# Kernel optimization log

Hardware: AMD Instinct MI355X
Metric: run time of the kernel (lower is better)

Reference implementation:

```python
import jax, jax.numpy as jnp
import numpy as np

STRIDES = (8, 16, 32)
FMP = ((160, 160), (80, 80), (40, 40))
NUM_CLASSES = 80
TOPK = 1000
CONF_THRESH = 0.05
NMS_THRESH = 0.6
IMG_MAX = 1280.0
CLASS_OFFSET = 8192.0  # > any box coordinate, separates classes for batched NMS


def setup_inputs() -> dict:
    key = jax.random.key(0)
    ks = jax.random.split(key, 32)
    C = 256
    inp = {}
    for l, (h, w) in enumerate(FMP):
        inp[f'feat{l}'] = jax.random.normal(ks[l], (1, C, h, w), dtype=jnp.float32)
        inp[f'Wobj{l}'] = jax.random.normal(ks[3 + 6 * l + 0], (1, C), dtype=jnp.float32) * 0.05
        inp[f'bobj{l}'] = jnp.zeros((1,), dtype=jnp.float32)
        inp[f'Wcls{l}'] = jax.random.normal(ks[3 + 6 * l + 2], (NUM_CLASSES, C), dtype=jnp.float32) * 0.05
        inp[f'bcls{l}'] = jnp.zeros((NUM_CLASSES,), dtype=jnp.float32)
        inp[f'Wreg{l}'] = jax.random.normal(ks[3 + 6 * l + 4], (4, C), dtype=jnp.float32) * 0.05
        inp[f'breg{l}'] = jnp.zeros((4,), dtype=jnp.float32)
    return inp


def _level(feat, Wo, bo, Wc, bc, Wr, br, stride):
    x = feat[0]  # [C,H,W]
    H, W = x.shape[1], x.shape[2]
    def conv1x1(Wm, bv):
        # 1x1 conv == channel GEMM; output [H*W, O]
        return (jnp.einsum('oc,chw->hwo', Wm, x) + bv).reshape(H * W, -1)
    obj = conv1x1(Wo, bo)              # [M,1]
    cls = conv1x1(Wc, bc)              # [M,C]
    reg = jnp.exp(conv1x1(Wr, br)) * stride  # [M,4] (l,t,r,b)
    prob = jax.nn.sigmoid(obj) * jax.nn.sigmoid(cls)
    scores = prob.max(axis=-1)
    labels = prob.argmax(axis=-1)
    ay, ax = jnp.meshgrid(jnp.arange(H), jnp.arange(W), indexing='ij')
    anchors = (jnp.stack([ax, ay], axis=-1).astype(jnp.float32).reshape(-1, 2) + 0.5) * stride
    k = min(TOPK, H * W)
    scores, idx = jax.lax.top_k(scores, k)
    labels = labels[idx]
    reg = reg[idx]
    anchors = anchors[idx]
    boxes = jnp.concatenate([anchors - reg[:, :2], anchors + reg[:, 2:]], axis=-1)
    return scores, labels, boxes


def _batched_nms(boxes, scores, labels):
    N = boxes.shape[0]
    valid = scores >= CONF_THRESH
    # class-offset trick: per-class NMS == single NMS on disjoint offset boxes
    ob = boxes + labels.astype(boxes.dtype)[:, None] * CLASS_OFFSET
    order = jnp.argsort(-scores)
    b = ob[order]
    v = valid[order]
    x1, y1, x2, y2 = b[:, 0], b[:, 1], b[:, 2], b[:, 3]
    areas = (x2 - x1) * (y2 - y1)
    xx1 = jnp.maximum(x1[:, None], x1[None, :])
    yy1 = jnp.maximum(y1[:, None], y1[None, :])
    xx2 = jnp.minimum(x2[:, None], x2[None, :])
    yy2 = jnp.minimum(y2[:, None], y2[None, :])
    w = jnp.maximum(1e-10, xx2 - xx1)
    h = jnp.maximum(1e-10, yy2 - yy1)
    inter = w * h
    iou = inter / (areas[:, None] + areas[None, :] - inter + 1e-14)
    idxs = jnp.arange(N)
    def body(i, keep):
        sup = keep[i] & (iou[i] > NMS_THRESH) & (idxs > i)
        return keep & ~sup
    keep_sorted = jax.lax.fori_loop(0, N, body, v)
    keep = jnp.zeros(N, dtype=bool).at[order].set(keep_sorted)
    return keep


def reference(feat0, feat1, feat2,
              Wobj0, bobj0, Wcls0, bcls0, Wreg0, breg0,
              Wobj1, bobj1, Wcls1, bcls1, Wreg1, breg1,
              Wobj2, bobj2, Wcls2, bcls2, Wreg2, breg2):
    feats = (feat0, feat1, feat2)
    params = ((Wobj0, bobj0, Wcls0, bcls0, Wreg0, breg0),
              (Wobj1, bobj1, Wcls1, bcls1, Wreg1, breg1),
              (Wobj2, bobj2, Wcls2, bcls2, Wreg2, breg2))
    ss, ll, bb = [], [], []
    for l in range(3):
        s, lab, box = _level(feats[l], *params[l], STRIDES[l])
        ss.append(s); ll.append(lab); bb.append(box)
    scores = jnp.concatenate(ss)
    labels = jnp.concatenate(ll)
    boxes = jnp.concatenate(bb)
    keep = _batched_nms(boxes, scores, labels)
    bboxes = jnp.clip(boxes / IMG_MAX, 0.0, 1.0)
    return bboxes, scores, labels.astype(jnp.int32), keep
```

## Files before the change

kernel.cpp:

```cpp
#include <hip/hip_runtime.h>
#include <math.h>

#define NTOT   33600
#define NSEL   3000
#define CAND_CAP 8192
#define NWORDS 47
#define NROWS_PAD 3008
#define FCAP 4

struct P21 {
  const float* feat[3];
  const float* Wobj[3];
  const float* bobj[3];
  const float* Wcls[3];
  const float* bcls[3];
  const float* Wreg[3];
  const float* breg[3];
};

__device__ __forceinline__ void level_of_block(int b, int t, int& l, int& p, int& g,
                                               int& HW, int& Wd, double& stride) {
  if (b < 100)      { l = 0; p = b * 256 + t;         g = p;          HW = 25600; Wd = 160; stride = 8.0;  }
  else if (b < 125) { l = 1; p = (b - 100) * 256 + t; g = 25600 + p;  HW = 6400;  Wd = 80;  stride = 16.0; }
  else              { l = 2; p = (b - 125) * 256 + t; g = 32000 + p;  HW = 1600;  Wd = 40;  stride = 32.0; }
}

__device__ __forceinline__ double sigmoid_d(double x) { return 1.0 / (1.0 + exp(-x)); }

__device__ __forceinline__ unsigned long long shfl64(unsigned long long v, int src) {
  unsigned lo = (unsigned)__shfl((int)(unsigned)(v & 0xFFFFFFFFull), src, 64);
  unsigned hi = (unsigned)__shfl((int)(unsigned)(v >> 32), src, 64);
  return (((unsigned long long)hi) << 32) | (unsigned long long)lo;
}

__global__ __launch_bounds__(256) void k_conv_chunk(P21 P,
    double* __restrict__ obj_t, double* __restrict__ reg_t,
    double* __restrict__ cmax, int* __restrict__ clab) {
  int l, p, g, HW, Wd; double stride;
  level_of_block(blockIdx.x, threadIdx.x, l, p, g, HW, Wd, stride);
  if (p >= HW) return;
  const int chunk = blockIdx.y;
  const float* __restrict__ fp = P.feat[l] + p;

  if (chunk == 0) {
    const float* __restrict__ Wobj = P.Wobj[l];
    const float* __restrict__ Wreg = P.Wreg[l];
    double accO = (double)P.bobj[l][0];
    double accR[4];
#pragma unroll
    for (int j = 0; j < 4; j++) accR[j] = (double)P.breg[l][j];
    for (int c = 0; c < 256; c += 8) {
      double xc[8];
#pragma unroll
      for (int u = 0; u < 8; u++) xc[u] = (double)fp[(c + u) * HW];
#pragma unroll
      for (int u = 0; u < 8; u++) {
        accO = fma((double)Wobj[c + u], xc[u], accO);
#pragma unroll
        for (int j = 0; j < 4; j++)
          accR[j] = fma((double)Wreg[j * 256 + c + u], xc[u], accR[j]);
      }
    }
    obj_t[g] = accO;
#pragma unroll
    for (int j = 0; j < 4; j++) reg_t[4 * g + j] = accR[j];
  } else {
    const int base = (chunk - 1) * 16;
    const float* __restrict__ Wcls = P.Wcls[l];
    const float* __restrict__ bcls = P.bcls[l];
    double a[16];
#pragma unroll
    for (int j = 0; j < 16; j++) a[j] = (double)bcls[base + j];
    for (int c = 0; c < 256; c += 8) {
      double xc[8];
#pragma unroll
      for (int u = 0; u < 8; u++) xc[u] = (double)fp[(c + u) * HW];
#pragma unroll
      for (int u = 0; u < 8; u++) {
#pragma unroll
        for (int j = 0; j < 16; j++)
          a[j] = fma((double)Wcls[(base + j) * 256 + c + u], xc[u], a[j]);
      }
    }
    double maxv = a[0]; int lab = base;
#pragma unroll
    for (int j = 1; j < 16; j++) if (a[j] > maxv) { maxv = a[j]; lab = base + j; }
    cmax[(chunk - 1) * NTOT + g] = maxv;
    clab[(chunk - 1) * NTOT + g] = lab;
  }
}

__global__ __launch_bounds__(256) void k_combine(
    const double* __restrict__ obj_t, const double* __restrict__ reg_t,
    const double* __restrict__ cmax, const int* __restrict__ clab,
    double* __restrict__ score_d, int* __restrict__ label_d,
    double* __restrict__ box_d, unsigned* __restrict__ hist) {
  int l, p, g, HW, Wd; double stride;
  level_of_block(blockIdx.x, threadIdx.x, l, p, g, HW, Wd, stride);
  if (p >= HW) return;

  double maxv = cmax[g]; int lab = clab[g];
#pragma unroll
  for (int k = 1; k < 5; k++) {
    double v = cmax[k * NTOT + g];
    int lb = clab[k * NTOT + g];
    if (v > maxv) { maxv = v; lab = lb; }
  }
  double score = sigmoid_d(obj_t[g]) * sigmoid_d(maxv);
  int h = p / Wd, w = p - h * Wd;
  double ax = ((double)w + 0.5) * stride;
  double ay = ((double)h + 0.5) * stride;
  double e0 = exp(reg_t[4 * g + 0]) * stride;
  double e1 = exp(reg_t[4 * g + 1]) * stride;
  double e2 = exp(reg_t[4 * g + 2]) * stride;
  double e3 = exp(reg_t[4 * g + 3]) * stride;

  score_d[g] = score;
  label_d[g] = lab;
  box_d[4 * g + 0] = ax - e0;
  box_d[4 * g + 1] = ay - e1;
  box_d[4 * g + 2] = ax + e2;
  box_d[4 * g + 3] = ay + e3;

  unsigned key = __float_as_uint((float)score);
  atomicAdd(&hist[l * 65536 + (key >> 16)], 1u);
}

__global__ __launch_bounds__(256) void k_scan(const unsigned* __restrict__ hist,
                                              unsigned* __restrict__ cutB) {
  int l = blockIdx.x;
  const unsigned* h = hist + l * 65536;
  __shared__ unsigned cs[256];
  __shared__ unsigned hb[256];
  __shared__ int s_chunk;
  __shared__ unsigned s_acc;
  int t = threadIdx.x;
  unsigned s = 0;
  for (int b = 0; b < 256; b++) s += h[t * 256 + b];
  cs[t] = s;
  __syncthreads();
  if (t == 0) {
    unsigned acc = 0; int chunk = 0;
    for (int tt = 255; tt >= 0; tt--) {
      if (acc + cs[tt] >= 1000u) { chunk = tt; break; }
      acc += cs[tt];
    }
    s_chunk = chunk; s_acc = acc;
  }
  __syncthreads();
  int chunk = s_chunk;
  hb[t] = h[chunk * 256 + t];
  __syncthreads();
  if (t == 0) {
    unsigned acc = s_acc;
    unsigned B = (unsigned)(chunk * 256);
    for (int b = 255; b >= 0; b--) {
      unsigned c = hb[b];
      if (acc + c >= 1000u) { B = (unsigned)(chunk * 256 + b); break; }
      acc += c;
    }
    cutB[l] = B;
  }
}

__global__ __launch_bounds__(256) void k_compact(const double* __restrict__ score_d,
    const unsigned* __restrict__ cutB, unsigned* __restrict__ cnt,
    double* __restrict__ cand_s, int* __restrict__ cand_g) {
  int l, p, g, HW, Wd; double stride;
  level_of_block(blockIdx.x, threadIdx.x, l, p, g, HW, Wd, stride);
  if (p >= HW) return;
  double sc = score_d[g];
  unsigned key = __float_as_uint((float)sc);
  if ((key >> 16) >= cutB[l]) {
    unsigned pos = atomicAdd(&cnt[l], 1u);
    if (pos < CAND_CAP) {
      cand_s[l * CAND_CAP + pos] = sc;
      cand_g[l * CAND_CAP + pos] = g;
    }
  }
}

__global__ __launch_bounds__(256) void k_rank(const double* __restrict__ cand_s,
    const int* __restrict__ cand_g, const unsigned* __restrict__ cnt,
    const int* __restrict__ label_d, const double* __restrict__ box_d,
    double* __restrict__ sel_s, int* __restrict__ sel_lab, double* __restrict__ sel_box) {
  const int l = blockIdx.y;
  const int M = (int)min(cnt[l], (unsigned)CAND_CAP);
  if (blockIdx.x * 4 >= M) return;
  const int q = blockIdx.x * 4 + (threadIdx.x >> 6);
  const int lane = threadIdx.x & 63;
  const bool active = (q < M);

  double s = 0.0; int g = 0;
  if (active) { s = cand_s[l * CAND_CAP + q]; g = cand_g[l * CAND_CAP + q]; }

  int r = 0;
  if (active) {
    for (int j = lane; j < M; j += 64) {
      double sj = cand_s[l * CAND_CAP + j];
      int gj = cand_g[l * CAND_CAP + j];
      r += (sj > s) || (sj == s && gj < g);
    }
  }
#pragma unroll
  for (int off = 32; off > 0; off >>= 1) r += __shfl_down(r, off, 64);

  if (active && lane == 0 && r < 1000) {
    int o = l * 1000 + r;
    sel_s[o] = s;
    sel_lab[o] = label_d[g];
    sel_box[4 * o + 0] = box_d[4 * g + 0];
    sel_box[4 * o + 1] = box_d[4 * g + 1];
    sel_box[4 * o + 2] = box_d[4 * g + 2];
    sel_box[4 * o + 3] = box_d[4 * g + 3];
  }
}

__global__ __launch_bounds__(256) void k_order(const double* __restrict__ sel_s,
                                               int* __restrict__ sortIdx) {
  const int i = blockIdx.x;
  const int t = threadIdx.x;
  const double s = sel_s[i];
  int r = 0;
  for (int j = t; j < NSEL; j += 256) {
    double sj = sel_s[j];
    r += (sj > s) || (sj == s && j < i);
  }
#pragma unroll
  for (int off = 32; off > 0; off >>= 1) r += __shfl_down(r, off, 64);
  __shared__ int wsum[4];
  if ((t & 63) == 0) wsum[t >> 6] = r;
  __syncthreads();
  if (t == 0) sortIdx[wsum[0] + wsum[1] + wsum[2] + wsum[3]] = i;
}

__global__ __launch_bounds__(256) void k_build(const double* __restrict__ sel_s,
    const int* __restrict__ sel_lab, const double* __restrict__ sel_box,
    const int* __restrict__ sortIdx, double* __restrict__ sbox, int* __restrict__ svalid) {
  int r = blockIdx.x * 256 + threadIdx.x;
  if (r >= NSEL) return;
  int i = sortIdx[r];
  double off = (double)sel_lab[i] * 8192.0;
  sbox[4 * r + 0] = sel_box[4 * i + 0] + off;
  sbox[4 * r + 1] = sel_box[4 * i + 1] + off;
  sbox[4 * r + 2] = sel_box[4 * i + 2] + off;
  sbox[4 * r + 3] = sel_box[4 * i + 3] + off;
  svalid[r] = (sel_s[i] >= 0.05) ? 1 : 0;
}

__global__ __launch_bounds__(64) void k_mask(const double* __restrict__ sbox,
    unsigned long long* __restrict__ denseG, unsigned long long* __restrict__ diagG,
    unsigned short* __restrict__ entG, unsigned short* __restrict__ cntG) {
  int i = blockIdx.x;
  int lane = threadIdx.x;
  double x1 = sbox[4 * i + 0], y1 = sbox[4 * i + 1];
  double x2 = sbox[4 * i + 2], y2 = sbox[4 * i + 3];
  double ar = (x2 - x1) * (y2 - y1);
  int iw = i >> 6;
  unsigned long long myw = 0ull, dg = 0ull;
  int cnt = 0;
  for (int w = 0; w < NWORDS; w++) {
    int j = w * 64 + lane;
    bool c = false;
    if (j < NSEL && j > i) {
      double bx1 = sbox[4 * j + 0], by1 = sbox[4 * j + 1];
      double bx2 = sbox[4 * j + 2], by2 = sbox[4 * j + 3];
      double arj = (bx2 - bx1) * (by2 - by1);
      double xx1 = fmax(x1, bx1), yy1 = fmax(y1, by1);
      double xx2 = fmin(x2, bx2), yy2 = fmin(y2, by2);
      double ww = fmax(1e-10, xx2 - xx1);
      double hh = fmax(1e-10, yy2 - yy1);
      double inter = ww * hh;
      double iou = inter / (ar + arj - inter + 1e-14);
      c = iou > 0.6;
    }
    unsigned long long word = __ballot(c);
    if (lane == w) myw = word;
    if (w == iw) dg = word;
    if (w > iw && lane == 0) {
      unsigned long long t = word;
      while (t) {
        int b = __builtin_ctzll(t); t &= t - 1;
        if (cnt < FCAP) entG[i * FCAP + cnt] = (unsigned short)(w * 64 + b);
        cnt++;
      }
    }
  }
  if (lane < NWORDS) denseG[(size_t)i * 48 + lane] = myw;
  if (lane == 0) { diagG[i] = dg; cntG[i] = (unsigned short)cnt; }
}

__global__ __launch_bounds__(256) void k_nms_scan(
    const unsigned long long* __restrict__ denseG, const unsigned long long* __restrict__ diagG,
    const unsigned short* __restrict__ entG, const unsigned short* __restrict__ cntG,
    const int* __restrict__ svalid, const int* __restrict__ sortIdx,
    int* __restrict__ keepOrig) {
  __shared__ unsigned long long diagL[NROWS_PAD];
  __shared__ unsigned short entL[NROWS_PAD * FCAP];
  __shared__ unsigned short cntL[NROWS_PAD];
  __shared__ unsigned long long validL[48];
  __shared__ unsigned long long hasWL[48];
  const int t = threadIdx.x;
  const int lane = t & 63;

  for (int i = t; i < NROWS_PAD; i += 256) {
    diagL[i] = (i < NSEL) ? diagG[i] : 0ull;
    cntL[i]  = (i < NSEL) ? cntG[i] : (unsigned short)0;
  }
  for (int k = t; k < NSEL * FCAP; k += 256) entL[k] = entG[k];
  for (int k = t + NSEL * FCAP; k < NROWS_PAD * FCAP; k += 256) entL[k] = 0;
  for (int i0 = t; i0 < NROWS_PAD; i0 += 256) {
    bool f = (i0 < NSEL) && (svalid[i0] != 0);
    unsigned long long b = __ballot(f);
    if ((t & 63) == 0) validL[i0 >> 6] = b;
  }
  __syncthreads();
  if (t >= 64) return;

  for (int w = 0; w < NWORDS; w++) {
    int i = w * 64 + lane;
    bool f = (diagL[i] != 0ull) || (cntL[i] != 0);
    unsigned long long b = __ballot(f);
    if (lane == 0) hasWL[w] = b;
  }

  unsigned long long rem = 0ull;
  unsigned long long keep = 0ull;
  for (int w = 0; w < NWORDS; w++) {
    unsigned long long vw = validL[w];
    unsigned long long remw = shfl64(rem, w);
    unsigned long long win = vw & ~remw;
    unsigned long long work = hasWL[w];
    while (work) {
      int d = __builtin_ctzll(work); work &= work - 1;
      if ((win >> d) & 1ull) {
        int i = w * 64 + d;
        win &= ~diagL[i];
        int c = cntL[i];
        if (c > FCAP) {
          unsigned long long rowj = (lane < NWORDS) ? denseG[(size_t)i * 48 + lane] : 0ull;
          rem |= rowj;
        } else {
          for (int k = 0; k < c; k++) {
            int j = entL[i * FCAP + k];
            if ((j >> 6) == lane) rem |= 1ull << (j & 63);
          }
        }
      }
    }
    if (lane == w) keep = win;
  }
  if (lane < NWORDS) {
    for (int b = 0; b < 64; b++) {
      int j = lane * 64 + b;
      if (j < NSEL) keepOrig[sortIdx[j]] = (int)((keep >> b) & 1ull);
    }
  }
}

__global__ __launch_bounds__(256) void k_out(const double* __restrict__ sel_s,
    const int* __restrict__ sel_lab, const double* __restrict__ sel_box,
    const int* __restrict__ keepOrig, float* __restrict__ out) {
  int i = blockIdx.x * 256 + threadIdx.x;
  if (i >= NSEL) return;
#pragma unroll
  for (int c = 0; c < 4; c++) {
    double v = sel_box[4 * i + c] / 1280.0;
    v = fmin(fmax(v, 0.0), 1.0);
    out[4 * i + c] = (float)v;
  }
  out[12000 + i] = (float)sel_s[i];
  out[15000 + i] = (float)sel_lab[i];
  out[18000 + i] = keepOrig[i] ? 1.0f : 0.0f;
}

extern "C" void kernel_launch(void* const* d_in, const int* in_sizes, int n_in,
                              void* d_out, int out_size, void* d_ws, size_t ws_size,
                              hipStream_t stream) {
  P21 P;
  for (int l = 0; l < 3; l++) {
    P.feat[l] = (const float*)d_in[7 * l + 0];
    P.Wobj[l] = (const float*)d_in[7 * l + 1];
    P.bobj[l] = (const float*)d_in[7 * l + 2];
    P.Wcls[l] = (const float*)d_in[7 * l + 3];
    P.bcls[l] = (const float*)d_in[7 * l + 4];
    P.Wreg[l] = (const float*)d_in[7 * l + 5];
    P.breg[l] = (const float*)d_in[7 * l + 6];
  }

  char* ws = (char*)d_ws;
  size_t off = 0;
  auto alloc = [&](size_t bytes) -> char* {
    char* p = ws + off;
    off += (bytes + 15) & ~(size_t)15;
    return p;
  };
  double* score_d  = (double*)alloc((size_t)NTOT * 8);
  double* box_d    = (double*)alloc((size_t)NTOT * 4 * 8);
  int*    label_d  = (int*)   alloc((size_t)NTOT * 4);
  double* obj_t    = (double*)alloc((size_t)NTOT * 8);
  double* reg_t    = (double*)alloc((size_t)NTOT * 4 * 8);
  double* cmax     = (double*)alloc((size_t)5 * NTOT * 8);
  int*    clab     = (int*)   alloc((size_t)5 * NTOT * 4);
  double* sel_s    = (double*)alloc((size_t)NSEL * 8);
  double* sel_box  = (double*)alloc((size_t)NSEL * 4 * 8);
  int*    sel_lab  = (int*)   alloc((size_t)NSEL * 4);
  int*    sortIdx  = (int*)   alloc((size_t)NSEL * 4);
  double* sbox     = (double*)alloc((size_t)NSEL * 4 * 8);
  int*    svalid   = (int*)   alloc((size_t)NSEL * 4);
  int*    keepOrig = (int*)   alloc((size_t)NSEL * 4);
  double* cand_s   = (double*)alloc((size_t)3 * CAND_CAP * 8);
  int*    cand_g   = (int*)   alloc((size_t)3 * CAND_CAP * 4);
  unsigned long long* denseG = (unsigned long long*)alloc((size_t)NSEL * 48 * 8);
  unsigned long long* diagG  = (unsigned long long*)alloc((size_t)NSEL * 8);
  unsigned short*     entG   = (unsigned short*)alloc((size_t)NSEL * FCAP * 2);
  unsigned short*     cntG   = (unsigned short*)alloc((size_t)NSEL * 2);
  unsigned* hist   = (unsigned*)alloc((size_t)3 * 65536 * 4);
  unsigned* cnt    = (unsigned*)alloc(16);
  unsigned* cutB   = (unsigned*)alloc(16);

  hipMemsetAsync(hist, 0, (size_t)3 * 65536 * 4 + 16, stream);

  dim3 cgrid(132, 6, 1);
  k_conv_chunk<<<cgrid, 256, 0, stream>>>(P, obj_t, reg_t, cmax, clab);
  k_combine <<<132, 256, 0, stream>>>(obj_t, reg_t, cmax, clab, score_d, label_d, box_d, hist);
  k_scan    <<<3, 256, 0, stream>>>(hist, cutB);
  k_compact <<<132, 256, 0, stream>>>(score_d, cutB, cnt, cand_s, cand_g);
  dim3 rgrid(CAND_CAP / 4, 3, 1);
  k_rank    <<<rgrid, 256, 0, stream>>>(cand_s, cand_g, cnt, label_d, box_d,
                                        sel_s, sel_lab, sel_box);
  k_order   <<<NSEL, 256, 0, stream>>>(sel_s, sortIdx);
  k_build   <<<(NSEL + 255) / 256, 256, 0, stream>>>(sel_s, sel_lab, sel_box, sortIdx, sbox, svalid);
  k_mask    <<<NSEL, 64, 0, stream>>>(sbox, denseG, diagG, entG, cntG);
  k_nms_scan<<<1, 256, 0, stream>>>(denseG, diagG, entG, cntG, svalid, sortIdx, keepOrig);
  k_out     <<<(NSEL + 255) / 256, 256, 0, stream>>>(sel_s, sel_lab, sel_box, keepOrig, (float*)d_out);
}
```

Baseline: 302.4 us.

## Split channel reduction across waves, parallelize histogram scan and IoU mask rows

The 1x1-conv kernel now gives each block 64 pixels and splits the 256 channels across four waves, reducing partial sums through shared memory. This gives 4x more blocks so more of the GPU is busy. The histogram memset is folded into the conv kernel and the serial per-thread histogram scan becomes a parallel wave-reduction kernel. The NMS mask kernel uses four waves per row. The nms_scan loads are vectorized. Risks are extra shared-memory sync and reduction overhead, and summation order changing from sequential to four partial sums, which could flip near-tie argmax or top-k results.

```diff
diff --git a/kernel.cpp b/kernel.cpp
--- a/kernel.cpp
+++ b/kernel.cpp
@@ -7,6 +7,8 @@
 #define NWORDS 47
 #define NROWS_PAD 3008
 #define FCAP 4
+#define NGRP 525
+#define HISTZ_N 196612
 
 struct P21 {
   const float* feat[3];
@@ -18,11 +20,11 @@
   const float* breg[3];
 };
 
-__device__ __forceinline__ void level_of_block(int b, int t, int& l, int& p, int& g,
+__device__ __forceinline__ void level_of_group(int grp, int lane, int& l, int& p, int& g,
                                                int& HW, int& Wd, double& stride) {
-  if (b < 100)      { l = 0; p = b * 256 + t;         g = p;          HW = 25600; Wd = 160; stride = 8.0;  }
-  else if (b < 125) { l = 1; p = (b - 100) * 256 + t; g = 25600 + p;  HW = 6400;  Wd = 80;  stride = 16.0; }
-  else              { l = 2; p = (b - 125) * 256 + t; g = 32000 + p;  HW = 1600;  Wd = 40;  stride = 32.0; }
+  if (grp < 400)      { l = 0; p = grp * 64 + lane;         g = p;         HW = 25600; Wd = 160; stride = 8.0;  }
+  else if (grp < 500) { l = 1; p = (grp - 400) * 64 + lane; g = 25600 + p; HW = 6400;  Wd = 80;  stride = 16.0; }
+  else                { l = 2; p = (grp - 500) * 64 + lane; g = 32000 + p; HW = 1600;  Wd = 40;  stride = 32.0; }
 }
 
 __device__ __forceinline__ double sigmoid_d(double x) { return 1.0 / (1.0 + exp(-x)); }
@@ -33,45 +35,59 @@
   return (((unsigned long long)hi) << 32) | (unsigned long long)lo;
 }
 
-__global__ __launch_bounds__(256) void k_conv_chunk(P21 P,
+__global__ __launch_bounds__(256) void k_conv(P21 P,
     double* __restrict__ obj_t, double* __restrict__ reg_t,
-    double* __restrict__ cmax, int* __restrict__ clab) {
+    double* __restrict__ cmax, int* __restrict__ clab,
+    unsigned* __restrict__ histz) {
+  __shared__ double sRed[4 * 16 * 64];
+  const int t = threadIdx.x, lane = t & 63, wk = t >> 6;
+  const int chunk = blockIdx.y;
   int l, p, g, HW, Wd; double stride;
-  level_of_block(blockIdx.x, threadIdx.x, l, p, g, HW, Wd, stride);
-  if (p >= HW) return;
-  const int chunk = blockIdx.y;
+  level_of_group(blockIdx.x, lane, l, p, g, HW, Wd, stride);
   const float* __restrict__ fp = P.feat[l] + p;
+  const int c0 = wk * 64;
 
   if (chunk == 0) {
+    for (int zi = blockIdx.x * 256 + t; zi < HISTZ_N; zi += NGRP * 256) histz[zi] = 0;
+
     const float* __restrict__ Wobj = P.Wobj[l];
     const float* __restrict__ Wreg = P.Wreg[l];
-    double accO = (double)P.bobj[l][0];
-    double accR[4];
-#pragma unroll
-    for (int j = 0; j < 4; j++) accR[j] = (double)P.breg[l][j];
-    for (int c = 0; c < 256; c += 8) {
+    double acc[5];
+    acc[0] = (wk == 0) ? (double)P.bobj[l][0] : 0.0;
+#pragma unroll
+    for (int j = 0; j < 4; j++) acc[1 + j] = (wk == 0) ? (double)P.breg[l][j] : 0.0;
+    for (int c = c0; c < c0 + 64; c += 8) {
       double xc[8];
 #pragma unroll
       for (int u = 0; u < 8; u++) xc[u] = (double)fp[(c + u) * HW];
 #pragma unroll
       for (int u = 0; u < 8; u++) {
-        accO = fma((double)Wobj[c + u], xc[u], accO);
+        acc[0] = fma((double)Wobj[c + u], xc[u], acc[0]);
 #pragma unroll
         for (int j = 0; j < 4; j++)
-          accR[j] = fma((double)Wreg[j * 256 + c + u], xc[u], accR[j]);
-      }
-    }
-    obj_t[g] = accO;
-#pragma unroll
-    for (int j = 0; j < 4; j++) reg_t[4 * g + j] = accR[j];
+          acc[1 + j] = fma((double)Wreg[j * 256 + c + u], xc[u], acc[1 + j]);
+      }
+    }
+#pragma unroll
+    for (int j = 0; j < 5; j++) sRed[(wk * 16 + j) * 64 + lane] = acc[j];
+    __syncthreads();
+    if (wk == 0) {
+#pragma unroll
+      for (int j = 0; j < 5; j++) {
+        double v = ((sRed[j * 64 + lane] + sRed[(16 + j) * 64 + lane])
+                    + sRed[(32 + j) * 64 + lane]) + sRed[(48 + j) * 64 + lane];
+        if (j == 0) obj_t[g] = v;
+        else        reg_t[4 * g + (j - 1)] = v;
+      }
+    }
   } else {
     const int base = (chunk - 1) * 16;
     const float* __restrict__ Wcls = P.Wcls[l];
     const float* __restrict__ bcls = P.bcls[l];
     double a[16];
 #pragma unroll
-    for (int j = 0; j < 16; j++) a[j] = (double)bcls[base + j];
-    for (int c = 0; c < 256; c += 8) {
+    for (int j = 0; j < 16; j++) a[j] = (wk == 0) ? (double)bcls[base + j] : 0.0;
+    for (int c = c0; c < c0 + 64; c += 8) {
       double xc[8];
 #pragma unroll
       for (int u = 0; u < 8; u++) xc[u] = (double)fp[(c + u) * HW];
@@ -82,22 +98,37 @@
           a[j] = fma((double)Wcls[(base + j) * 256 + c + u], xc[u], a[j]);
       }
     }
-    double maxv = a[0]; int lab = base;
-#pragma unroll
-    for (int j = 1; j < 16; j++) if (a[j] > maxv) { maxv = a[j]; lab = base + j; }
-    cmax[(chunk - 1) * NTOT + g] = maxv;
-    clab[(chunk - 1) * NTOT + g] = lab;
-  }
-}
-
-__global__ __launch_bounds__(256) void k_combine(
+#pragma unroll
+    for (int j = 0; j < 16; j++) sRed[(wk * 16 + j) * 64 + lane] = a[j];
+    __syncthreads();
+#pragma unroll
+    for (int jj = 0; jj < 4; jj++) {
+      int j = wk * 4 + jj;
+      double v = ((sRed[j * 64 + lane] + sRed[(16 + j) * 64 + lane])
+                  + sRed[(32 + j) * 64 + lane]) + sRed[(48 + j) * 64 + lane];
+      sRed[j * 64 + lane] = v;
+    }
+    __syncthreads();
+    if (wk == 0) {
+      double maxv = sRed[lane]; int lab = base;
+#pragma unroll
+      for (int j = 1; j < 16; j++) {
+        double v = sRed[j * 64 + lane];
+        if (v > maxv) { maxv = v; lab = base + j; }
+      }
+      cmax[(chunk - 1) * NTOT + g] = maxv;
+      clab[(chunk - 1) * NTOT + g] = lab;
+    }
+  }
+}
+
+__global__ __launch_bounds__(64) void k_combine(
     const double* __restrict__ obj_t, const double* __restrict__ reg_t,
     const double* __restrict__ cmax, const int* __restrict__ clab,
     double* __restrict__ score_d, int* __restrict__ label_d,
     double* __restrict__ box_d, unsigned* __restrict__ hist) {
   int l, p, g, HW, Wd; double stride;
-  level_of_block(blockIdx.x, threadIdx.x, l, p, g, HW, Wd, stride);
-  if (p >= HW) return;
+  level_of_group(blockIdx.x, threadIdx.x, l, p, g, HW, Wd, stride);
 
   double maxv = cmax[g]; int lab = clab[g];
 #pragma unroll
@@ -126,18 +157,28 @@
   atomicAdd(&hist[l * 65536 + (key >> 16)], 1u);
 }
 
-__global__ __launch_bounds__(256) void k_scan(const unsigned* __restrict__ hist,
-                                              unsigned* __restrict__ cutB) {
+__global__ __launch_bounds__(256) void k_scan_a(const unsigned* __restrict__ hist,
+                                                unsigned* __restrict__ csG) {
+  const int lane = threadIdx.x & 63;
+  const int row = blockIdx.x * 4 + (threadIdx.x >> 6);
+  const uint4* hp = (const uint4*)(hist + row * 256);
+  uint4 v = hp[lane];
+  unsigned s = v.x + v.y + v.z + v.w;
+#pragma unroll
+  for (int off = 32; off > 0; off >>= 1) s += (unsigned)__shfl_down((int)s, off, 64);
+  if (lane == 0) csG[row] = s;
+}
+
+__global__ __launch_bounds__(256) void k_scan_b(const unsigned* __restrict__ hist,
+                                                const unsigned* __restrict__ csG,
+                                                unsigned* __restrict__ cutB) {
   int l = blockIdx.x;
-  const unsigned* h = hist + l * 65536;
   __shared__ unsigned cs[256];
   __shared__ unsigned hb[256];
   __shared__ int s_chunk;
   __shared__ unsigned s_acc;
   int t = threadIdx.x;
-  unsigned s = 0;
-  for (int b = 0; b < 256; b++) s += h[t * 256 + b];
-  cs[t] = s;
+  cs[t] = csG[l * 256 + t];
   __syncthreads();
   if (t == 0) {
     unsigned acc = 0; int chunk = 0;
@@ -149,7 +190,7 @@
   }
   __syncthreads();
   int chunk = s_chunk;
-  hb[t] = h[chunk * 256 + t];
+  hb[t] = hist[l * 65536 + chunk * 256 + t];
   __syncthreads();
   if (t == 0) {
     unsigned acc = s_acc;
@@ -163,12 +204,11 @@
   }
 }
 
-__global__ __launch_bounds__(256) void k_compact(const double* __restrict__ score_d,
+__global__ __launch_bounds__(64) void k_compact(const double* __restrict__ score_d,
     const unsigned* __restrict__ cutB, unsigned* __restrict__ cnt,
     double* __restrict__ cand_s, int* __restrict__ cand_g) {
   int l, p, g, HW, Wd; double stride;
-  level_of_block(blockIdx.x, threadIdx.x, l, p, g, HW, Wd, stride);
-  if (p >= HW) return;
+  level_of_group(blockIdx.x, threadIdx.x, l, p, g, HW, Wd, stride);
   double sc = score_d[g];
   unsigned key = __float_as_uint((float)sc);
   if ((key >> 16) >= cutB[l]) {
@@ -248,18 +288,21 @@
   svalid[r] = (sel_s[i] >= 0.05) ? 1 : 0;
 }
 
-__global__ __launch_bounds__(64) void k_mask(const double* __restrict__ sbox,
+__global__ __launch_bounds__(256) void k_mask(const double* __restrict__ sbox,
     unsigned long long* __restrict__ denseG, unsigned long long* __restrict__ diagG,
     unsigned short* __restrict__ entG, unsigned short* __restrict__ cntG) {
-  int i = blockIdx.x;
-  int lane = threadIdx.x;
-  double x1 = sbox[4 * i + 0], y1 = sbox[4 * i + 1];
-  double x2 = sbox[4 * i + 2], y2 = sbox[4 * i + 3];
-  double ar = (x2 - x1) * (y2 - y1);
-  int iw = i >> 6;
-  unsigned long long myw = 0ull, dg = 0ull;
-  int cnt = 0;
-  for (int w = 0; w < NWORDS; w++) {
+  __shared__ unsigned long long wordS[48];
+  __shared__ unsigned short entS[FCAP];
+  __shared__ int cntS;
+  const int i = blockIdx.x;
+  const int t = threadIdx.x, lane = t & 63, wk = t >> 6;
+  if (t == 0) cntS = 0;
+  const double x1 = sbox[4 * i + 0], y1 = sbox[4 * i + 1];
+  const double x2 = sbox[4 * i + 2], y2 = sbox[4 * i + 3];
+  const double ar = (x2 - x1) * (y2 - y1);
+  const int iw = i >> 6;
+  __syncthreads();
+  for (int w = wk; w < NWORDS; w += 4) {
     int j = w * 64 + lane;
     bool c = false;
     if (j < NSEL && j > i) {
@@ -275,19 +318,28 @@
       c = iou > 0.6;
     }
     unsigned long long word = __ballot(c);
-    if (lane == w) myw = word;
-    if (w == iw) dg = word;
-    if (w > iw && lane == 0) {
-      unsigned long long t = word;
-      while (t) {
-        int b = __builtin_ctzll(t); t &= t - 1;
-        if (cnt < FCAP) entG[i * FCAP + cnt] = (unsigned short)(w * 64 + b);
-        cnt++;
-      }
-    }
-  }
-  if (lane < NWORDS) denseG[(size_t)i * 48 + lane] = myw;
-  if (lane == 0) { diagG[i] = dg; cntG[i] = (unsigned short)cnt; }
+    if (lane == 0) {
+      wordS[w] = word;
+      if (w > iw && word) {
+        unsigned long long tt = word;
+        while (tt) {
+          int b = __builtin_ctzll(tt); tt &= tt - 1;
+          int slot = atomicAdd(&cntS, 1);
+          if (slot < FCAP) entS[slot] = (unsigned short)(w * 64 + b);
+        }
+      }
+    }
+  }
+  __syncthreads();
+  if (t < NWORDS) denseG[(size_t)i * 48 + t] = wordS[t];
+  if (t == 0) {
+    diagG[i] = wordS[iw];
+    int c = cntS;
+    cntG[i] = (unsigned short)c;
+    int cs = c < FCAP ? c : FCAP;
+    for (int k = 0; k < cs; k++) entG[i * FCAP + k] = entS[k];
+    for (int k = cs; k < FCAP; k++) entG[i * FCAP + k] = 0;
+  }
 }
 
 __global__ __launch_bounds__(256) void k_nms_scan(
@@ -303,12 +355,14 @@
   const int t = threadIdx.x;
   const int lane = t & 63;
 
-  for (int i = t; i < NROWS_PAD; i += 256) {
-    diagL[i] = (i < NSEL) ? diagG[i] : 0ull;
-    cntL[i]  = (i < NSEL) ? cntG[i] : (unsigned short)0;
-  }
-  for (int k = t; k < NSEL * FCAP; k += 256) entL[k] = entG[k];
-  for (int k = t + NSEL * FCAP; k < NROWS_PAD * FCAP; k += 256) entL[k] = 0;
+  for (int k = t; k < NSEL; k += 256) diagL[k] = diagG[k];
+  for (int k = NSEL + t; k < NROWS_PAD; k += 256) diagL[k] = 0ull;
+  uint2* e2 = (uint2*)entL; const uint2* eg2 = (const uint2*)entG;
+  for (int k = t; k < NSEL; k += 256) e2[k] = eg2[k];
+  for (int k = NSEL + t; k < NROWS_PAD; k += 256) { uint2 z; z.x = 0; z.y = 0; e2[k] = z; }
+  unsigned* c2 = (unsigned*)cntL; const unsigned* cg2 = (const unsigned*)cntG;
+  for (int k = t; k < NSEL / 2; k += 256) c2[k] = cg2[k];
+  for (int k = NSEL / 2 + t; k < NROWS_PAD / 2; k += 256) c2[k] = 0;
   for (int i0 = t; i0 < NROWS_PAD; i0 += 256) {
     bool f = (i0 < NSEL) && (svalid[i0] != 0);
     unsigned long long b = __ballot(f);
@@ -418,20 +472,20 @@
   unsigned* hist   = (unsigned*)alloc((size_t)3 * 65536 * 4);
   unsigned* cnt    = (unsigned*)alloc(16);
   unsigned* cutB   = (unsigned*)alloc(16);
-
-  hipMemsetAsync(hist, 0, (size_t)3 * 65536 * 4 + 16, stream);
-
-  dim3 cgrid(132, 6, 1);
-  k_conv_chunk<<<cgrid, 256, 0, stream>>>(P, obj_t, reg_t, cmax, clab);
-  k_combine <<<132, 256, 0, stream>>>(obj_t, reg_t, cmax, clab, score_d, label_d, box_d, hist);
-  k_scan    <<<3, 256, 0, stream>>>(hist, cutB);
-  k_compact <<<132, 256, 0, stream>>>(score_d, cutB, cnt, cand_s, cand_g);
+  unsigned* csG    = (unsigned*)alloc((size_t)768 * 4);
+
+  dim3 cgrid(NGRP, 6, 1);
+  k_conv    <<<cgrid, 256, 0, stream>>>(P, obj_t, reg_t, cmax, clab, hist);
+  k_combine <<<NGRP, 64, 0, stream>>>(obj_t, reg_t, cmax, clab, score_d, label_d, box_d, hist);
+  k_scan_a  <<<192, 256, 0, stream>>>(hist, csG);
+  k_scan_b  <<<3, 256, 0, stream>>>(hist, csG, cutB);
+  k_compact <<<NGRP, 64, 0, stream>>>(score_d, cutB, cnt, cand_s, cand_g);
   dim3 rgrid(CAND_CAP / 4, 3, 1);
   k_rank    <<<rgrid, 256, 0, stream>>>(cand_s, cand_g, cnt, label_d, box_d,
                                         sel_s, sel_lab, sel_box);
   k_order   <<<NSEL, 256, 0, stream>>>(sel_s, sortIdx);
   k_build   <<<(NSEL + 255) / 256, 256, 0, stream>>>(sel_s, sel_lab, sel_box, sortIdx, sbox, svalid);
-  k_mask    <<<NSEL, 64, 0, stream>>>(sbox, denseG, diagG, entG, cntG);
+  k_mask    <<<NSEL, 256, 0, stream>>>(sbox, denseG, diagG, entG, cntG);
   k_nms_scan<<<1, 256, 0, stream>>>(denseG, diagG, entG, cntG, svalid, sortIdx, keepOrig);
   k_out     <<<(NSEL + 255) / 256, 256, 0, stream>>>(sel_s, sel_lab, sel_box, keepOrig, (float*)d_out);
 }
```

Result: slower. 390.8 us (+29.2%).
